# Kernel optimization log

Measured on AMD Instinct MI355X. Metric: run time of the kernel, lower is better.

Reference implementation:

```python
import jax, jax.numpy as jnp
import numpy as np
import math

B, T, F, H, C = 512, 26, 2048, 1024, 22


def _lstm_cell(x_t, h, c, Wih, Whh, bih, bhh):
    # PyTorch gate order: i, f, g, o. Gates: [B, 4H]
    gates = x_t @ Wih.T + h @ Whh.T + bih + bhh
    i, f, g, o = jnp.split(gates, 4, axis=-1)
    c_new = jax.nn.sigmoid(f) * c + jax.nn.sigmoid(i) * jnp.tanh(g)
    h_new = jax.nn.sigmoid(o) * jnp.tanh(c_new)
    return h_new, c_new


def setup_inputs() -> dict:
    key = jax.random.key(0)
    ks = jax.random.split(key, 13)
    s_enc = 1.0 / math.sqrt(H)
    inp = {
        "x": jax.random.normal(ks[0], (B, T, F), jnp.float32),
        "enc_Wih": jax.random.normal(ks[1], (4 * H, F), jnp.float32) * s_enc,
        "enc_Whh": jax.random.normal(ks[2], (4 * H, H), jnp.float32) * s_enc,
        "enc_bih": jax.random.normal(ks[3], (4 * H,), jnp.float32) * s_enc,
        "enc_bhh": jax.random.normal(ks[4], (4 * H,), jnp.float32) * s_enc,
        "proj_W": jax.random.normal(ks[5], (H, H), jnp.float32) * s_enc,
        "proj_b": jax.random.normal(ks[6], (H,), jnp.float32) * s_enc,
        "dec_Wih": jax.random.normal(ks[7], (4 * H, H + F), jnp.float32) * s_enc,
        "dec_Whh": jax.random.normal(ks[8], (4 * H, H), jnp.float32) * s_enc,
        "dec_bih": jax.random.normal(ks[9], (4 * H,), jnp.float32) * s_enc,
        "dec_bhh": jax.random.normal(ks[10], (4 * H,), jnp.float32) * s_enc,
        "cls_W": jax.random.normal(ks[11], (C, H), jnp.float32) * s_enc,
        "cls_b": jax.random.normal(ks[12], (C,), jnp.float32) * s_enc,
    }
    return inp


def reference(x, enc_Wih, enc_Whh, enc_bih, enc_bhh, proj_W, proj_b,
              dec_Wih, dec_Whh, dec_bih, dec_bhh, cls_W, cls_b):
    # feature_extractor treated as identity (fusion_size == F)
    b, t, _ = x.shape
    h = x.shape[-1]  # noqa (F)

    # ---- Encoder LSTM over time (batch_first) ----
    def enc_step(carry, x_t):
        h_prev, c_prev = carry
        h_new, c_new = _lstm_cell(x_t, h_prev, c_prev, enc_Wih, enc_Whh, enc_bih, enc_bhh)
        return (h_new, c_new), h_new

    h0 = jnp.zeros((b, H), x.dtype)
    c0 = jnp.zeros((b, H), x.dtype)
    xs = jnp.swapaxes(x, 0, 1)  # [T, B, F]
    _, h_ts = jax.lax.scan(enc_step, (h0, c0), xs)  # [T, B, H]
    h_ts = jnp.swapaxes(h_ts, 0, 1)  # [B, T, H]

    proj_h_ts = h_ts @ proj_W.T + proj_b  # [B, T, H]
    inv_sqrt_h = 1.0 / math.sqrt(H)

    # ---- Decoder with per-step attention ----
    def dec_step(carry, x_t):
        dec_h, dec_c = carry
        # attention scores over encoder timesteps
        attn_logits = jnp.einsum('bh,bth->bt', dec_h, proj_h_ts) * inv_sqrt_h
        attn_w = jax.nn.softmax(attn_logits, axis=-1)
        attn = jnp.einsum('bt,bth->bh', attn_w, proj_h_ts)  # [B, H]
        inp_t = jnp.concatenate([x_t, attn], axis=1)  # [B, F+H]
        dec_h, dec_c = _lstm_cell(inp_t, dec_h, dec_c, dec_Wih, dec_Whh, dec_bih, dec_bhh)
        score = dec_h @ cls_W.T + cls_b  # [B, C]
        return (dec_h, dec_c), score

    _, scores = jax.lax.scan(dec_step, (h0, c0), xs)  # [T, B, C]
    return jnp.swapaxes(scores, 0, 1)  # [B, T, C]
```

## Files before the change

### kernel.cpp

```cpp
#include <hip/hip_runtime.h>

#define DB 512
#define DT 26
#define DF 2048
#define DH 1024
#define DG 4096
#define DC 22

typedef unsigned short u16;
typedef u16 u16x8 __attribute__((ext_vector_type(8)));
typedef __bf16 bf16x8 __attribute__((ext_vector_type(8)));
typedef float f32x4 __attribute__((ext_vector_type(4)));

__device__ __forceinline__ float sigm(float x) { return 1.f / (1.f + __expf(-x)); }

__device__ __forceinline__ u16 f2b(float v) {
  unsigned u = __float_as_uint(v);
  return (u16)((u + 0x7FFFu + ((u >> 16) & 1u)) >> 16);
}
__device__ __forceinline__ float b2f(u16 h) {
  return __uint_as_float(((unsigned)h) << 16);
}
__device__ __forceinline__ void store_b4(u16* __restrict__ d, size_t o, float4 v) {
  ushort4 s;
  s.x = f2b(v.x); s.y = f2b(v.y); s.z = f2b(v.z); s.w = f2b(v.w);
  *(ushort4*)(d + o) = s;
}

template <int OUTBF>
__global__ __launch_bounds__(256) void gemm_bt(
    const u16* __restrict__ A1, long lda1, int K1,
    const u16* __restrict__ A2, long lda2,
    const u16* __restrict__ B, long ldb, const float* __restrict__ bias,
    void* __restrict__ Cp, long ldc, int M, int N, int K)
{
  constexpr int LR = 72;
  __shared__ __align__(16) u16 sA[64 * LR];
  __shared__ __align__(16) u16 sB[128 * LR];
  const int tid = threadIdx.x, lane = tid & 63;
  const int wid = tid >> 6, wm = wid >> 1, wn = wid & 1;
  const int nbm = M >> 6;
  const int cpx = gridDim.x >> 3;
  const int swz = (blockIdx.x & 7) * cpx + (blockIdx.x >> 3);
  const int bn = swz / nbm, bm = swz % nbm;
  const size_t m0 = (size_t)bm << 6, n0 = (size_t)bn << 7;

  const int row = tid >> 3, c8 = tid & 7;
  u16x8 ra[2], rb[4];

  auto loadA = [&](int k0) {
    const u16* p; long lda; int kk;
    if (k0 < K1) { p = A1; lda = lda1; kk = k0; }
    else         { p = A2; lda = lda2; kk = k0 - K1; }
#pragma unroll
    for (int r = 0; r < 2; ++r)
      ra[r] = *(const u16x8*)(p + (m0 + row + r * 32) * (size_t)lda + (size_t)(kk + c8 * 8));
  };
  auto loadB = [&](int k0) {
#pragma unroll
    for (int r = 0; r < 4; ++r)
      rb[r] = *(const u16x8*)(B + (n0 + row + r * 32) * (size_t)ldb + (size_t)(k0 + c8 * 8));
  };
  loadA(0);
  loadB(0);

  f32x4 acc[2][4] = {};
  for (int k0 = 0; k0 < K; k0 += 64) {
    __syncthreads();
#pragma unroll
    for (int r = 0; r < 2; ++r) *(u16x8*)(sA + (row + r * 32) * LR + c8 * 8) = ra[r];
#pragma unroll
    for (int r = 0; r < 4; ++r) *(u16x8*)(sB + (row + r * 32) * LR + c8 * 8) = rb[r];
    __syncthreads();
    if (k0 + 64 < K) { loadA(k0 + 64); loadB(k0 + 64); }
#pragma unroll
    for (int ks = 0; ks < 2; ++ks) {
      const int ko = ks * 32 + (lane >> 4) * 8;
      bf16x8 af[2], bfr[4];
#pragma unroll
      for (int mi = 0; mi < 2; ++mi)
        af[mi] = *(const bf16x8*)(sA + ((wm << 5) + (mi << 4) + (lane & 15)) * LR + ko);
#pragma unroll
      for (int ni = 0; ni < 4; ++ni)
        bfr[ni] = *(const bf16x8*)(sB + ((wn << 6) + (ni << 4) + (lane & 15)) * LR + ko);
#pragma unroll
      for (int mi = 0; mi < 2; ++mi)
#pragma unroll
        for (int ni = 0; ni < 4; ++ni)
          acc[mi][ni] = __builtin_amdgcn_mfma_f32_16x16x32_bf16(af[mi], bfr[ni], acc[mi][ni], 0, 0, 0);
    }
  }

#pragma unroll
  for (int mi = 0; mi < 2; ++mi) {
    const int row0 = (wm << 5) + (mi << 4) + ((lane >> 4) << 2);
#pragma unroll
    for (int ni = 0; ni < 4; ++ni) {
      const size_t gn = n0 + (size_t)((wn << 6) + (ni << 4) + (lane & 15));
      const float bv = bias[gn];
#pragma unroll
      for (int r = 0; r < 4; ++r) {
        const size_t gm = m0 + (size_t)(row0 + r);
        const float v = acc[mi][ni][r] + bv;
        if (OUTBF) ((u16*)Cp)[gm * (size_t)ldc + gn] = f2b(v);
        else       ((float*)Cp)[gm * (size_t)ldc + gn] = v;
      }
    }
  }
}

template <int DEC>
__global__ __launch_bounds__(512) void step_gemm(
    const u16* __restrict__ A, const u16* __restrict__ B,
    const u16* __restrict__ xg, long ldxg, float* __restrict__ cst,
    u16* __restrict__ hout, int K, int first)
{
  constexpr int LR = 72;
  __shared__ __align__(16) u16 sA[64 * LR];
  __shared__ __align__(16) u16 sB[128 * LR];
  const int tid = threadIdx.x, lane = tid & 63;
  const int wid = tid >> 6, wm = wid >> 1, wn = wid & 1;
  const int cpx = gridDim.x >> 3;
  const int swz = (blockIdx.x & 7) * cpx + (blockIdx.x >> 3);
  const int bn = swz >> 3, bm = swz & 7;
  const size_t m0 = (size_t)bm << 6, n0 = (size_t)bn << 7;

  const int row = tid >> 3, c8 = tid & 7;
  u16x8 ra, rb[2];
  auto loadA = [&](int k0) {
    ra = *(const u16x8*)(A + (m0 + row) * (size_t)K + (size_t)(k0 + c8 * 8));
  };
  auto loadB = [&](int k0) {
#pragma unroll
    for (int r = 0; r < 2; ++r)
      rb[r] = *(const u16x8*)(B + (n0 + row + r * 64) * (size_t)K + (size_t)(k0 + c8 * 8));
  };
  loadA(0);
  loadB(0);

  f32x4 acc[4] = {};
  for (int k0 = 0; k0 < K; k0 += 64) {
    __syncthreads();
    *(u16x8*)(sA + row * LR + c8 * 8) = ra;
#pragma unroll
    for (int r = 0; r < 2; ++r) *(u16x8*)(sB + (row + r * 64) * LR + c8 * 8) = rb[r];
    __syncthreads();
    if (k0 + 64 < K) { loadA(k0 + 64); loadB(k0 + 64); }
#pragma unroll
    for (int ks = 0; ks < 2; ++ks) {
      const int ko = ks * 32 + (lane >> 4) * 8;
      bf16x8 af, bfr[4];
      af = *(const bf16x8*)(sA + ((wm << 4) + (lane & 15)) * LR + ko);
#pragma unroll
      for (int ni = 0; ni < 4; ++ni)
        bfr[ni] = *(const bf16x8*)(sB + ((wn << 6) + (ni << 4) + (lane & 15)) * LR + ko);
#pragma unroll
      for (int ni = 0; ni < 4; ++ni)
        acc[ni] = __builtin_amdgcn_mfma_f32_16x16x32_bf16(af, bfr[ni], acc[ni], 0, 0, 0);
    }
  }

  const int l = lane & 15;
  const int hg = (bn << 5) + (wn << 4) + l;
  const int row0 = (wm << 4) + ((lane >> 4) << 2);
#pragma unroll
  for (int r = 0; r < 4; ++r) {
    const int gm = (int)m0 + row0 + r;
    const u16* xr = xg + (size_t)gm * ldxg + n0 + (wn << 6) + l;
    const float gi = acc[0][r] + b2f(xr[0]);
    const float gf = acc[1][r] + b2f(xr[16]);
    const float gg = acc[2][r] + b2f(xr[32]);
    const float go = acc[3][r] + b2f(xr[48]);
    const size_t ch = ((size_t)gm << 10) + hg;
    const float cp = first ? 0.f : cst[ch];
    const float cn = sigm(gf) * cp + sigm(gi) * tanhf(gg);
    const float hn = sigm(go) * tanhf(cn);
    cst[ch] = cn;
    if (DEC) hout[((size_t)gm << 11) + 1024 + hg] = f2b(hn);
    else     hout[((size_t)gm << 10) + hg] = f2b(hn);
  }
}

__global__ __launch_bounds__(256) void cvt4_kernel(const float* __restrict__ src,
    u16* __restrict__ dst, int n4) {
  for (int i = blockIdx.x * 256 + threadIdx.x; i < n4; i += gridDim.x * 256) {
    float4 v = *(const float4*)(src + (size_t)i * 4);
    store_b4(dst, (size_t)i * 4, v);
  }
}

__global__ __launch_bounds__(256) void pack_perm_kernel(const float* __restrict__ src,
    long ld_src, long scol, int cols4, u16* __restrict__ dst, long ld_dst, long dcol) {
  const int total = DG * cols4;
  for (int i = blockIdx.x * 256 + threadIdx.x; i < total; i += gridDim.x * 256) {
    const int np = i / cols4, c4 = i - np * cols4;
    const int g = (np >> 4) & 3, h = ((np >> 6) << 4) | (np & 15);
    const int n = g * 1024 + h;
    float4 v = *(const float4*)(src + (size_t)n * ld_src + scol + (size_t)c4 * 4);
    store_b4(dst, (size_t)np * ld_dst + dcol + (size_t)c4 * 4, v);
  }
}

__global__ void pack_bias_perm_kernel(const float* __restrict__ a,
    const float* __restrict__ b, float* __restrict__ o) {
  int np = blockIdx.x * 256 + threadIdx.x;
  if (np < DG) {
    const int g = (np >> 4) & 3, h = ((np >> 6) << 4) | (np & 15);
    const int n = g * 1024 + h;
    o[np] = a[n] + b[n];
  }
}

template <int DO_ATTN>
__global__ __launch_bounds__(256) void attn_cls_kernel(
    const u16* __restrict__ projH, const u16* __restrict__ Zr, u16* __restrict__ Zw,
    const float* __restrict__ clsW, const float* __restrict__ clsb,
    float* __restrict__ out, int do_cls, int tprev)
{
  const int b = blockIdx.x, tid = threadIdx.x, lane = tid & 63, wid = tid >> 6;
  __shared__ float redc[DC][4];
  __shared__ float red[DT][4];
  __shared__ float wgt[DT];

  ushort4 hz = *(const ushort4*)(Zr + ((size_t)b << 11) + 1024 + tid * 4);
  float4 hv = make_float4(b2f(hz.x), b2f(hz.y), b2f(hz.z), b2f(hz.w));

  if (do_cls) {
    float acc[DC];
#pragma unroll
    for (int c = 0; c < DC; ++c) {
      const float4 w = *(const float4*)(clsW + ((size_t)c << 10) + tid * 4);
      acc[c] = hv.x * w.x + hv.y * w.y + hv.z * w.z + hv.w * w.w;
    }
#pragma unroll
    for (int c = 0; c < DC; ++c) {
      float v = acc[c];
#pragma unroll
      for (int off = 32; off; off >>= 1) v += __shfl_xor(v, off);
      if (lane == 0) redc[c][wid] = v;
    }
  }

  if (DO_ATTN) {
    float ph[DT][4];
    float p[DT];
#pragma unroll
    for (int t = 0; t < DT; ++t) {
      ushort4 pv = *(const ushort4*)(projH + (((size_t)t * DB + b) << 10) + tid * 4);
      ph[t][0] = b2f(pv.x); ph[t][1] = b2f(pv.y); ph[t][2] = b2f(pv.z); ph[t][3] = b2f(pv.w);
      p[t] = hv.x * ph[t][0] + hv.y * ph[t][1] + hv.z * ph[t][2] + hv.w * ph[t][3];
    }
#pragma unroll
    for (int t = 0; t < DT; ++t) {
#pragma unroll
      for (int off = 32; off; off >>= 1) p[t] += __shfl_xor(p[t], off);
      if (lane == 0) red[t][wid] = p[t];
    }
    __syncthreads();
    if (tid == 0) {
      float lg[DT];
      float mx = -1e30f;
#pragma unroll
      for (int t = 0; t < DT; ++t) {
        lg[t] = (red[t][0] + red[t][1] + red[t][2] + red[t][3]) * 0.03125f;
        mx = fmaxf(mx, lg[t]);
      }
      float s = 0.f;
#pragma unroll
      for (int t = 0; t < DT; ++t) { lg[t] = __expf(lg[t] - mx); s += lg[t]; }
      float inv = 1.f / s;
#pragma unroll
      for (int t = 0; t < DT; ++t) wgt[t] = lg[t] * inv;
    }
    __syncthreads();
    float4 a = make_float4(0, 0, 0, 0);
#pragma unroll
    for (int t = 0; t < DT; ++t) {
      const float w = wgt[t];
      a.x += w * ph[t][0]; a.y += w * ph[t][1]; a.z += w * ph[t][2]; a.w += w * ph[t][3];
    }
    store_b4(Zw, ((size_t)b << 11) + tid * 4, a);
  }

  if (do_cls) {
    __syncthreads();
    if (tid < DC)
      out[((size_t)b * DT + tprev) * DC + tid] =
          redc[tid][0] + redc[tid][1] + redc[tid][2] + redc[tid][3] + clsb[tid];
  }
}

extern "C" void kernel_launch(void* const* d_in, const int* in_sizes, int n_in,
                              void* d_out, int out_size, void* d_ws, size_t ws_size,
                              hipStream_t stream) {
  const float* x    = (const float*)d_in[0];
  const float* eWih = (const float*)d_in[1];
  const float* eWhh = (const float*)d_in[2];
  const float* ebih = (const float*)d_in[3];
  const float* ebhh = (const float*)d_in[4];
  const float* pW   = (const float*)d_in[5];
  const float* pb   = (const float*)d_in[6];
  const float* dWih = (const float*)d_in[7];
  const float* dWhh = (const float*)d_in[8];
  const float* dbih = (const float*)d_in[9];
  const float* dbhh = (const float*)d_in[10];
  const float* clsW = (const float*)d_in[11];
  const float* clsb = (const float*)d_in[12];
  float* out = (float*)d_out;

  char* p = (char*)d_ws;
  auto alloc = [&](size_t bytes) -> void* {
    char* r = p; p += (bytes + 255) & ~(size_t)255; return (void*)r;
  };
  u16* Xb    = (u16*)alloc((size_t)DB * DT * DF * 2);
  u16* eWx   = (u16*)alloc((size_t)DG * 2048 * 2);
  u16* eWh   = (u16*)alloc((size_t)DG * 1024 * 2);
  u16* dWx   = (u16*)alloc((size_t)DG * 2048 * 2);
  u16* dWah  = (u16*)alloc((size_t)DG * 2048 * 2);
  u16* pWb   = (u16*)alloc((size_t)DH * DH * 2);
  u16* Hb    = (u16*)alloc((size_t)DT * DB * DH * 2);
  u16* encXg = (u16*)alloc((size_t)DB * DT * DG * 2);
  u16* decXg = (u16*)alloc((size_t)DB * DT * DG * 2);
  u16* Z0    = (u16*)alloc((size_t)DB * 2048 * 2);
  u16* Z1    = (u16*)alloc((size_t)DB * 2048 * 2);
  u16* Hz    = (u16*)alloc((size_t)DB * DH * 2);
  float* eCs = (float*)alloc((size_t)DB * DH * 4);
  float* dCs = (float*)alloc((size_t)DB * DH * 4);
  float* ebs = (float*)alloc(DG * 4);
  float* dbs = (float*)alloc(DG * 4);
  u16* projHb = Xb;

  cvt4_kernel<<<2048, 256, 0, stream>>>(x, Xb, (int)((size_t)DB * DT * DF / 4));
  pack_perm_kernel<<<2048, 256, 0, stream>>>(eWih, DF, 0, DF / 4, eWx, 2048, 0);
  pack_perm_kernel<<<2048, 256, 0, stream>>>(eWhh, DH, 0, DH / 4, eWh, 1024, 0);
  pack_perm_kernel<<<2048, 256, 0, stream>>>(dWih, 3072, 0, DF / 4, dWx, 2048, 0);
  pack_perm_kernel<<<2048, 256, 0, stream>>>(dWih, 3072, 2048, DH / 4, dWah, 2048, 0);
  pack_perm_kernel<<<2048, 256, 0, stream>>>(dWhh, DH, 0, DH / 4, dWah, 2048, 1024);
  cvt4_kernel<<<1024, 256, 0, stream>>>(pW, pWb, DH * DH / 4);
  pack_bias_perm_kernel<<<16, 256, 0, stream>>>(ebih, ebhh, ebs);
  pack_bias_perm_kernel<<<16, 256, 0, stream>>>(dbih, dbhh, dbs);
  hipMemsetAsync(Hz, 0, (size_t)DB * DH * 2, stream);
  hipMemsetAsync(Z0, 0, (size_t)DB * 2048 * 2, stream);

  gemm_bt<1><<<6656, 256, 0, stream>>>(
      Xb, DF, DF, Xb, DF, eWx, DF, ebs, encXg, DG, DB * DT, DG, DF);
  gemm_bt<1><<<6656, 256, 0, stream>>>(
      Xb, DF, DF, Xb, DF, dWx, DF, dbs, decXg, DG, DB * DT, DG, DF);

  for (int t = 0; t < DT; ++t) {
    step_gemm<0><<<256, 512, 0, stream>>>(
        (t == 0) ? Hz : (Hb + (size_t)(t - 1) * DB * DH), eWh,
        encXg + (size_t)t * DG, (long)DT * DG, eCs,
        Hb + (size_t)t * DB * DH, DH, t == 0);
  }

  gemm_bt<1><<<1664, 256, 0, stream>>>(
      Hb, DH, DH, Hb, DH, pWb, DH, pb, projHb, DH, DT * DB, DH, DH);

  for (int t = 0; t < DT; ++t) {
    u16* Zc = (t & 1) ? Z1 : Z0;
    u16* Zn = (t & 1) ? Z0 : Z1;
    attn_cls_kernel<1><<<DB, 256, 0, stream>>>(
        projHb, Zc, Zc, clsW, clsb, out, t > 0, t - 1);
    step_gemm<1><<<256, 512, 0, stream>>>(
        Zc, dWah, decXg + (size_t)t * DG, (long)DT * DG, dCs, Zn, 2048, t == 0);
  }
  attn_cls_kernel<0><<<DB, 256, 0, stream>>>(
      projHb, Z0, Z0, clsW, clsb, out, 1, DT - 1);
}
```

Baseline: 2.174 ms.

## Replace recurrent step GEMM with weight-panel kernel streaming A from global

The per-timestep LSTM recurrent GEMM is restructured. Each block now loads a full 64x1024 weight panel into LDS (about 132KB) once per phase and streams activation rows directly from global memory into MFMA fragments. This removes the per-64-K double sync loop, and the decoder runs two phases over the concatenated K. The bulk gemm_bt also swaps its block swizzle to be row-major over N tiles and uses nontemporal stores for outputs. The large LDS footprint limits occupancy to one block per CU, and A is read straight from global without LDS reuse.

```diff
diff --git a/kernel.cpp b/kernel.cpp
--- a/kernel.cpp
+++ b/kernel.cpp
@@ -39,10 +39,10 @@
   __shared__ __align__(16) u16 sB[128 * LR];
   const int tid = threadIdx.x, lane = tid & 63;
   const int wid = tid >> 6, wm = wid >> 1, wn = wid & 1;
-  const int nbm = M >> 6;
+  const int nbn = N >> 7;
   const int cpx = gridDim.x >> 3;
   const int swz = (blockIdx.x & 7) * cpx + (blockIdx.x >> 3);
-  const int bn = swz / nbm, bm = swz % nbm;
+  const int bm = swz / nbn, bn = swz % nbn;
   const size_t m0 = (size_t)bm << 6, n0 = (size_t)bn << 7;
 
   const int row = tid >> 3, c8 = tid & 7;
@@ -102,71 +102,69 @@
       for (int r = 0; r < 4; ++r) {
         const size_t gm = m0 + (size_t)(row0 + r);
         const float v = acc[mi][ni][r] + bv;
-        if (OUTBF) ((u16*)Cp)[gm * (size_t)ldc + gn] = f2b(v);
-        else       ((float*)Cp)[gm * (size_t)ldc + gn] = v;
+        if (OUTBF) __builtin_nontemporal_store(f2b(v), (u16*)Cp + gm * (size_t)ldc + gn);
+        else       __builtin_nontemporal_store(v, (float*)Cp + gm * (size_t)ldc + gn);
       }
     }
   }
 }
 
-template <int DEC>
-__global__ __launch_bounds__(512) void step_gemm(
-    const u16* __restrict__ A, const u16* __restrict__ B,
-    const u16* __restrict__ xg, long ldxg, float* __restrict__ cst,
-    u16* __restrict__ hout, int K, int first)
+template <int PHASES>
+__global__ __launch_bounds__(512) void step_panel(
+    const u16* __restrict__ A, long lda,
+    const u16* __restrict__ W, long ldw,
+    const u16* __restrict__ xg, long ldxg,
+    float* __restrict__ cst, u16* __restrict__ hout, long ldh, long hoff,
+    int first)
 {
-  constexpr int LR = 72;
-  __shared__ __align__(16) u16 sA[64 * LR];
-  __shared__ __align__(16) u16 sB[128 * LR];
-  const int tid = threadIdx.x, lane = tid & 63;
-  const int wid = tid >> 6, wm = wid >> 1, wn = wid & 1;
+  constexpr int LRP = 1032;
+  __shared__ __align__(16) u16 sB[64 * LRP];
+  const int tid = threadIdx.x, lane = tid & 63, w = tid >> 6;
   const int cpx = gridDim.x >> 3;
   const int swz = (blockIdx.x & 7) * cpx + (blockIdx.x >> 3);
-  const int bn = swz >> 3, bm = swz & 7;
-  const size_t m0 = (size_t)bm << 6, n0 = (size_t)bn << 7;
-
-  const int row = tid >> 3, c8 = tid & 7;
-  u16x8 ra, rb[2];
-  auto loadA = [&](int k0) {
-    ra = *(const u16x8*)(A + (m0 + row) * (size_t)K + (size_t)(k0 + c8 * 8));
-  };
-  auto loadB = [&](int k0) {
-#pragma unroll
-    for (int r = 0; r < 2; ++r)
-      rb[r] = *(const u16x8*)(B + (n0 + row + r * 64) * (size_t)K + (size_t)(k0 + c8 * 8));
-  };
-  loadA(0);
-  loadB(0);
+  const int nblk = swz >> 2, mg = swz & 3;
+  const int n0 = nblk << 6;
+  const int l15 = lane & 15, l4 = lane >> 4;
+  const int arow = mg * 128 + (w << 4) + l15;
+  const int kof = l4 * 8;
 
   f32x4 acc[4] = {};
-  for (int k0 = 0; k0 < K; k0 += 64) {
-    __syncthreads();
-    *(u16x8*)(sA + row * LR + c8 * 8) = ra;
-#pragma unroll
-    for (int r = 0; r < 2; ++r) *(u16x8*)(sB + (row + r * 64) * LR + c8 * 8) = rb[r];
-    __syncthreads();
-    if (k0 + 64 < K) { loadA(k0 + 64); loadB(k0 + 64); }
-#pragma unroll
-    for (int ks = 0; ks < 2; ++ks) {
-      const int ko = ks * 32 + (lane >> 4) * 8;
-      bf16x8 af, bfr[4];
-      af = *(const bf16x8*)(sA + ((wm << 4) + (lane & 15)) * LR + ko);
-#pragma unroll
-      for (int ni = 0; ni < 4; ++ni)
-        bfr[ni] = *(const bf16x8*)(sB + ((wn << 6) + (ni << 4) + (lane & 15)) * LR + ko);
-#pragma unroll
-      for (int ni = 0; ni < 4; ++ni)
-        acc[ni] = __builtin_amdgcn_mfma_f32_16x16x32_bf16(af, bfr[ni], acc[ni], 0, 0, 0);
-    }
-  }
-
-  const int l = lane & 15;
-  const int hg = (bn << 5) + (wn << 4) + l;
-  const int row0 = (wm << 4) + ((lane >> 4) << 2);
+#pragma unroll
+  for (int ph = 0; ph < PHASES; ++ph) {
+    if (ph) __syncthreads();
+#pragma unroll
+    for (int i = 0; i < 16; ++i) {
+      const int c = i * 512 + tid;
+      const int r = c >> 7, cc = c & 127;
+      *(u16x8*)(sB + r * LRP + cc * 8) =
+          *(const u16x8*)(W + (size_t)(n0 + r) * ldw + ph * 1024 + cc * 8);
+    }
+    __syncthreads();
+
+    const u16* Ap = A + (size_t)arow * lda + ph * 1024 + kof;
+    bf16x8 af = *(const bf16x8*)(Ap);
+#pragma unroll 2
+    for (int ko = 0; ko < 1024; ko += 32) {
+      bf16x8 afn = af;
+      if (ko + 32 < 1024) afn = *(const bf16x8*)(Ap + ko + 32);
+      bf16x8 b0 = *(const bf16x8*)(sB + (l15)      * LRP + ko + kof);
+      bf16x8 b1 = *(const bf16x8*)(sB + (16 + l15) * LRP + ko + kof);
+      bf16x8 b2 = *(const bf16x8*)(sB + (32 + l15) * LRP + ko + kof);
+      bf16x8 b3 = *(const bf16x8*)(sB + (48 + l15) * LRP + ko + kof);
+      acc[0] = __builtin_amdgcn_mfma_f32_16x16x32_bf16(af, b0, acc[0], 0, 0, 0);
+      acc[1] = __builtin_amdgcn_mfma_f32_16x16x32_bf16(af, b1, acc[1], 0, 0, 0);
+      acc[2] = __builtin_amdgcn_mfma_f32_16x16x32_bf16(af, b2, acc[2], 0, 0, 0);
+      acc[3] = __builtin_amdgcn_mfma_f32_16x16x32_bf16(af, b3, acc[3], 0, 0, 0);
+      af = afn;
+    }
+  }
+
+  const int hg = (nblk << 4) | l15;
+  const int row0 = mg * 128 + (w << 4) + (l4 << 2);
 #pragma unroll
   for (int r = 0; r < 4; ++r) {
-    const int gm = (int)m0 + row0 + r;
-    const u16* xr = xg + (size_t)gm * ldxg + n0 + (wn << 6) + l;
+    const int gm = row0 + r;
+    const u16* xr = xg + (size_t)gm * ldxg + n0 + l15;
     const float gi = acc[0][r] + b2f(xr[0]);
     const float gf = acc[1][r] + b2f(xr[16]);
     const float gg = acc[2][r] + b2f(xr[32]);
@@ -176,8 +174,7 @@
     const float cn = sigm(gf) * cp + sigm(gi) * tanhf(gg);
     const float hn = sigm(go) * tanhf(cn);
     cst[ch] = cn;
-    if (DEC) hout[((size_t)gm << 11) + 1024 + hg] = f2b(hn);
-    else     hout[((size_t)gm << 10) + hg] = f2b(hn);
+    hout[(size_t)gm * ldh + hoff + hg] = f2b(hn);
   }
 }
 
@@ -348,10 +345,11 @@
       Xb, DF, DF, Xb, DF, dWx, DF, dbs, decXg, DG, DB * DT, DG, DF);
 
   for (int t = 0; t < DT; ++t) {
-    step_gemm<0><<<256, 512, 0, stream>>>(
-        (t == 0) ? Hz : (Hb + (size_t)(t - 1) * DB * DH), eWh,
+    step_panel<1><<<256, 512, 0, stream>>>(
+        (t == 0) ? Hz : (Hb + (size_t)(t - 1) * DB * DH), DH,
+        eWh, 1024,
         encXg + (size_t)t * DG, (long)DT * DG, eCs,
-        Hb + (size_t)t * DB * DH, DH, t == 0);
+        Hb + (size_t)t * DB * DH, DH, 0, t == 0);
   }
 
   gemm_bt<1><<<1664, 256, 0, stream>>>(
@@ -362,8 +360,10 @@
     u16* Zn = (t & 1) ? Z0 : Z1;
     attn_cls_kernel<1><<<DB, 256, 0, stream>>>(
         projHb, Zc, Zc, clsW, clsb, out, t > 0, t - 1);
-    step_gemm<1><<<256, 512, 0, stream>>>(
-        Zc, dWah, decXg + (size_t)t * DG, (long)DT * DG, dCs, Zn, 2048, t == 0);
+    step_panel<2><<<256, 512, 0, stream>>>(
+        Zc, 2048, dWah, 2048,
+        decXg + (size_t)t * DG, (long)DT * DG, dCs,
+        Zn, 2048, 1024, t == 0);
   }
   attn_cls_kernel<0><<<DB, 256, 0, stream>>>(
       projHb, Z0, Z0, clsW, clsb, out, 1, DT - 1);
```

Measured after the change: 2.635 ms. +21.2%, slower.
